# Optimization experiments

Hardware: AMD Instinct MI355X
Metric: run time of the kernel (lower is better)

Reference implementation:

```python
import jax, jax.numpy as jnp
import numpy as np


def _bilinear_sample(fea, px, py):
    # fea: [C,H,W]; px,py: [D,H,W] pixel coords (align_corners=True, zeros padding)
    C, H, W = fea.shape
    x0 = jnp.floor(px); y0 = jnp.floor(py)
    wx = px - x0; wy = py - y0
    x0i = x0.astype(jnp.int32); y0i = y0.astype(jnp.int32)

    def g(xi, yi):
        valid = (xi >= 0) & (xi < W) & (yi >= 0) & (yi < H)
        v = fea[:, jnp.clip(yi, 0, H - 1), jnp.clip(xi, 0, W - 1)]  # [C,D,H,W]
        return jnp.where(valid[None], v, 0.0)

    return (g(x0i, y0i) * ((1 - wx) * (1 - wy))[None]
            + g(x0i + 1, y0i) * (wx * (1 - wy))[None]
            + g(x0i, y0i + 1) * ((1 - wx) * wy)[None]
            + g(x0i + 1, y0i + 1) * (wx * wy)[None])


def homo_warping_3d(src_fea, src_proj, ref_proj, depth_values):
    # src_fea [B,C,H,W]; src_proj/ref_proj [B,4,4]; depth_values [B,D] -> [B,C,D,H,W]
    B, C, H, W = src_fea.shape
    D = depth_values.shape[1]
    proj = src_proj @ jnp.linalg.inv(ref_proj)
    rot, trans = proj[:, :3, :3], proj[:, :3, 3]
    yy, xx = jnp.meshgrid(jnp.arange(H, dtype=src_fea.dtype),
                          jnp.arange(W, dtype=src_fea.dtype), indexing='ij')
    xyz = jnp.stack([xx.ravel(), yy.ravel(), jnp.ones(H * W, src_fea.dtype)], 0)  # [3,HW]
    rot_xyz = jnp.einsum('bij,jp->bip', rot, xyz)  # [B,3,HW]
    pxyz = rot_xyz[:, :, None, :] * depth_values[:, None, :, None] + trans[:, :, None, None]
    xy = pxyz[:, :2] / pxyz[:, 2:3]
    # grid is computed under torch.no_grad() in the original
    px = jax.lax.stop_gradient(xy[:, 0].reshape(B, D, H, W))
    py = jax.lax.stop_gradient(xy[:, 1].reshape(B, D, H, W))
    return jax.vmap(_bilinear_sample)(src_fea, px, py)  # [B,C,D,H,W]


def conf_regression(p, n=4):
    # sliding sum of n consecutive depth probabilities, gathered at expected depth index
    B, D, H, W = p.shape
    pad = jnp.pad(p, ((0, 0), (1, 2), (0, 0), (0, 0)))  # [B,D+3,H,W]
    cs = jnp.cumsum(pad, axis=1)
    cs = jnp.concatenate([jnp.zeros_like(cs[:, :1]), cs], axis=1)  # [B,D+4,H,W]
    sum_n = cs[:, n:n + D] - cs[:, 0:D]  # [B,D,H,W]
    d_idx = jnp.sum(p * jnp.arange(D, dtype=p.dtype)[None, :, None, None], axis=1)
    idx = jnp.clip(d_idx.astype(jnp.int32), 0, D - 1)
    return jnp.take_along_axis(sum_n, idx[:, None], axis=1)[:, 0]


def reference(ref_feats, src_feats, proj_matrices, depth_values, num_depth, w_reg):
    V = proj_matrices.shape[1]
    assert ref_feats.shape[0] == V - 1 and depth_values.shape[1] == num_depth
    ref_proj = proj_matrices[:, 0]
    ref_proj_new = ref_proj[:, 0].at[:, :3, :4].set(ref_proj[:, 1, :3, :3] @ ref_proj[:, 0, :3, :4])
    volume_sum = 0.0
    for v in range(V - 1):
        src_proj = proj_matrices[:, v + 1]
        src_proj_new = src_proj[:, 0].at[:, :3, :4].set(src_proj[:, 1, :3, :3] @ src_proj[:, 0, :3, :4])
        warped = homo_warping_3d(src_feats[v], src_proj_new, ref_proj_new, depth_values)
        volume_sum = volume_sum + ref_feats[v][:, :, None] * warped  # [B,C,D,H,W]
    volume_mean = volume_sum / (V - 1)
    # cost regularization: bias-free 3x3x3 3D conv C->1
    cost = jax.lax.conv_general_dilated(volume_mean, w_reg, (1, 1, 1), 'SAME',
                                        dimension_numbers=('NCDHW', 'OIDHW', 'NCDHW'))
    prob_volume = jax.nn.softmax(cost[:, 0], axis=1)  # [B,D,H,W]
    depth = jnp.sum(prob_volume * depth_values[:, :, None, None], axis=1)  # [B,H,W]
    conf = jax.lax.stop_gradient(conf_regression(prob_volume))  # [B,H,W]
    return depth, conf


def setup_inputs() -> dict:
    key = jax.random.key(0)
    B, V, C, D, H, W = 1, 5, 32, 48, 128, 160
    k1, k2, k3 = jax.random.split(key, 3)
    ref_feats = jax.random.normal(k1, (V - 1, B, C, H, W), jnp.float32)
    src_feats = jax.random.normal(k2, (V - 1, B, C, H, W), jnp.float32)
    # geometrically valid cameras: index 0 = extrinsic 4x4, index 1 = intrinsic 4x4
    f = 200.0
    K = np.eye(4, dtype=np.float32)
    K[0, 0] = f; K[1, 1] = f; K[0, 2] = W / 2.0; K[1, 2] = H / 2.0
    projs = np.zeros((B, V, 2, 4, 4), np.float32)
    for v in range(V):
        ang = 0.04 * v
        R = np.array([[np.cos(ang), 0, np.sin(ang)], [0, 1, 0], [-np.sin(ang), 0, np.cos(ang)]], np.float32)
        E = np.eye(4, dtype=np.float32)
        E[:3, :3] = R
        E[:3, 3] = np.array([-40.0 * v, 0.0, 0.0], np.float32)
        projs[:, v, 0] = E
        projs[:, v, 1] = K
    depth_values = jnp.broadcast_to(jnp.linspace(425.0, 935.0, D, dtype=jnp.float32)[None], (B, D))
    w_reg = jax.random.normal(k3, (1, C, 3, 3, 3), jnp.float32) * 0.05
    return {"ref_feats": ref_feats, "src_feats": src_feats,
            "proj_matrices": jnp.asarray(projs), "depth_values": depth_values,
            "num_depth": D, "w_reg": w_reg}
```

## Files before the change

kernel.cpp:

```cpp
#include <hip/hip_runtime.h>
#include <math.h>

#define H_ 128
#define W_ 160
#define D_ 48
#define C_ 32
#define K27 27
#define HW_ (H_ * W_)
#define DHW_ (D_ * HW_)
#define CHW_ (C_ * HW_)

typedef float f4 __attribute__((ext_vector_type(4)));

__device__ __forceinline__ void build_proj(const float* __restrict__ P, int v,
                                           double M[4][4]) {
    const float* E = P + (v * 2 + 0) * 16;
    const float* K = P + (v * 2 + 1) * 16;
    for (int i = 0; i < 3; i++)
        for (int j = 0; j < 4; j++) {
            double s = 0.0;
            for (int k = 0; k < 3; k++) s += (double)K[i * 4 + k] * (double)E[k * 4 + j];
            M[i][j] = s;
        }
    for (int j = 0; j < 4; j++) M[3][j] = (double)E[12 + j];
}

__device__ void do_proj(const float* __restrict__ P, float* __restrict__ rt) {
    double M0[4][4];
    build_proj(P, 0, M0);
    double a[4][8];
    for (int i = 0; i < 4; i++)
        for (int j = 0; j < 4; j++) {
            a[i][j] = M0[i][j];
            a[i][4 + j] = (i == j) ? 1.0 : 0.0;
        }
    for (int col = 0; col < 4; ++col) {
        int piv = col;
        double best = fabs(a[col][col]);
        for (int r = col + 1; r < 4; r++) {
            double vv = fabs(a[r][col]);
            if (vv > best) { best = vv; piv = r; }
        }
        if (piv != col)
            for (int j = 0; j < 8; j++) {
                double t = a[col][j]; a[col][j] = a[piv][j]; a[piv][j] = t;
            }
        double inv = 1.0 / a[col][col];
        for (int j = 0; j < 8; j++) a[col][j] *= inv;
        for (int r = 0; r < 4; r++)
            if (r != col) {
                double f = a[r][col];
                for (int j = 0; j < 8; j++) a[r][j] -= f * a[col][j];
            }
    }
    double Minv[4][4];
    for (int i = 0; i < 4; i++)
        for (int j = 0; j < 4; j++) Minv[i][j] = a[i][4 + j];

    for (int v = 1; v < 5; ++v) {
        double Mv[4][4];
        build_proj(P, v, Mv);
        double Pm[4][4];
        for (int i = 0; i < 4; i++)
            for (int j = 0; j < 4; j++) {
                double s = 0.0;
                for (int k = 0; k < 4; k++) s += Mv[i][k] * Minv[k][j];
                Pm[i][j] = s;
            }
        float* o = rt + (v - 1) * 12;
        o[0] = (float)Pm[0][0]; o[1] = (float)Pm[0][1]; o[2] = (float)Pm[0][2];
        o[3] = (float)Pm[1][0]; o[4] = (float)Pm[1][1]; o[5] = (float)Pm[1][2];
        o[6] = (float)Pm[2][0]; o[7] = (float)Pm[2][1]; o[8] = (float)Pm[2][2];
        o[9] = (float)Pm[0][3]; o[10] = (float)Pm[1][3]; o[11] = (float)Pm[2][3];
    }
}

__global__ void __launch_bounds__(256)
transpose2_kernel(const float* __restrict__ sf, const float* __restrict__ rf,
                  float* __restrict__ so, float* __restrict__ ro,
                  const float* __restrict__ P, float* __restrict__ rt) {
    int blk = blockIdx.x;
    if (blk >= 2560) {
        if (threadIdx.x == 0) do_proj(P, rt);
        return;
    }
    __shared__ float tile[C_][65];
    int t = threadIdx.x;
    int tv = blk / 320;
    int tileI = blk % 320;
    int pixbase = tileI * 64;
    const float* in = (tv < 4) ? sf : rf;
    float* out = (tv < 4) ? so : ro;
    int v = tv & 3;

    int pix = t & 63;
    int cbase = (t >> 6) * 8;
#pragma unroll
    for (int cc = 0; cc < 8; cc++) {
        int c = cbase + cc;
        tile[c][pix] = in[(size_t)v * CHW_ + c * HW_ + pixbase + pix];
    }
    __syncthreads();

    float* obase = out + ((size_t)v * HW_ + pixbase) * C_;
#pragma unroll
    for (int r = 0; r < 2; r++) {
        int i = r * 256 + t;
        int wpix = i >> 3;
        int c0 = (i & 7) * 4;
        f4 w = {tile[c0][wpix], tile[c0 + 1][wpix], tile[c0 + 2][wpix],
                tile[c0 + 3][wpix]};
        *(f4*)(obase + (size_t)wpix * C_ + c0) = w;
    }
}

__global__ void __launch_bounds__(256)
warp_fold_x_kernel(const float* __restrict__ srcT,
                   const float* __restrict__ refT,
                   const float* __restrict__ rt,
                   const float* __restrict__ dvals,
                   const float* __restrict__ wreg,
                   float* __restrict__ Gx) {
    __shared__ float accT[8][64][4];
    __shared__ float gLDS[K27][164];

    int t = threadIdx.x;
    int vox = t >> 2;
    int cgrp = t & 3;
    int blk = blockIdx.x;
    int d = blk >> 7;
    int y = blk & 127;
    float depth = dvals[d];
    float yf = (float)y;
    int rowbase = d * HW_ + y * W_;

#pragma unroll 1
    for (int b = 0; b < 3; b++) {
        int vg = b * 64 + vox;
        int x = vg - 1;

        f4 acc0 = (f4){0.f, 0.f, 0.f, 0.f};
        f4 acc1 = (f4){0.f, 0.f, 0.f, 0.f};

        if (x >= 0 && x < W_) {
            float xf = (float)x;
            int pix = y * W_ + x;
#pragma unroll 2
            for (int v = 0; v < 4; v++) {
                const float* m = rt + v * 12;
                float px = fmaf(fmaf(m[0], xf, fmaf(m[1], yf, m[2])), depth, m[9]);
                float py = fmaf(fmaf(m[3], xf, fmaf(m[4], yf, m[5])), depth, m[10]);
                float pz = fmaf(fmaf(m[6], xf, fmaf(m[7], yf, m[8])), depth, m[11]);
                float iz = 1.f / pz;
                px *= iz;
                py *= iz;
                float x0f = floorf(px), y0f = floorf(py);
                float wx = px - x0f, wy = py - y0f;
                int x0 = (int)x0f, y0 = (int)y0f;
                int x1 = x0 + 1, y1 = y0 + 1;

                float w00 = (1.f - wx) * (1.f - wy);
                float w10 = wx * (1.f - wy);
                float w01 = (1.f - wx) * wy;
                float w11 = wx * wy;
                bool vx0 = (x0 >= 0) && (x0 < W_);
                bool vx1 = (x1 >= 0) && (x1 < W_);
                bool vy0 = (y0 >= 0) && (y0 < H_);
                bool vy1 = (y1 >= 0) && (y1 < H_);
                if (!(vx0 && vy0)) w00 = 0.f;
                if (!(vx1 && vy0)) w10 = 0.f;
                if (!(vx0 && vy1)) w01 = 0.f;
                if (!(vx1 && vy1)) w11 = 0.f;
                int cx0 = min(max(x0, 0), W_ - 1);
                int cx1 = min(max(x1, 0), W_ - 1);
                int cy0 = min(max(y0, 0), H_ - 1);
                int cy1 = min(max(y1, 0), H_ - 1);

                const float* sv = srcT + (size_t)v * HW_ * C_ + cgrp * 8;
                const f4* p00 = (const f4*)(sv + (cy0 * W_ + cx0) * C_);
                const f4* p10 = (const f4*)(sv + (cy0 * W_ + cx1) * C_);
                const f4* p01 = (const f4*)(sv + (cy1 * W_ + cx0) * C_);
                const f4* p11 = (const f4*)(sv + (cy1 * W_ + cx1) * C_);
                const f4* pr  = (const f4*)(refT + ((size_t)v * HW_ + pix) * C_ + cgrp * 8);

                f4 a00 = p00[0], b00 = p00[1];
                f4 a10 = p10[0], b10 = p10[1];
                f4 a01 = p01[0], b01 = p01[1];
                f4 a11 = p11[0], b11 = p11[1];
                f4 r0 = pr[0],  r1 = pr[1];

                f4 sv0 = a00 * w00 + a10 * w10 + a01 * w01 + a11 * w11;
                f4 sv1 = b00 * w00 + b10 * w10 + b01 * w01 + b11 * w11;
                acc0 += r0 * sv0;
                acc1 += r1 * sv1;
            }
            acc0 *= 0.25f;
            acc1 *= 0.25f;
        }

        int cq0 = cgrp * 2;
        *(f4*)&accT[cq0][vox][0] = acc0;
        *(f4*)&accT[cq0 + 1][vox][0] = acc1;
        __syncthreads();

        int fvox = t & 63;
        int kg = t >> 6;
        int fvg = b * 64 + fvox;
        float av[C_];
#pragma unroll
        for (int cq = 0; cq < 8; cq++)
            *(f4*)&av[cq * 4] = *(const f4*)&accT[cq][fvox][0];

        if (fvg < 162) {
            int kstart = kg * 7;
            int kend = min(kstart + 7, K27);
#pragma unroll 1
            for (int k = kstart; k < kend; k++) {
                int ku = __builtin_amdgcn_readfirstlane(k);
                float g = 0.f;
#pragma unroll
                for (int c = 0; c < C_; c++) g = fmaf(wreg[c * K27 + ku], av[c], g);
                gLDS[ku][fvg] = g;
            }
        }
        __syncthreads();
    }

    if (t < W_) {
        int x = t;
#pragma unroll
        for (int j = 0; j < 9; j++) {
            float s = gLDS[j * 3 + 0][x] + gLDS[j * 3 + 1][x + 1] +
                      gLDS[j * 3 + 2][x + 2];
            Gx[(size_t)j * DHW_ + rowbase + x] = s;
        }
    }
}

__global__ void __launch_bounds__(512)
gather_softmax_kernel(const float* __restrict__ Gx,
                      const float* __restrict__ dvals,
                      float* __restrict__ out) {
    __shared__ float E[D_][64];
    __shared__ float red[8][64];
    __shared__ float sums[3][8][64];

    int t = threadIdx.x;
    int lx = t & 63;
    int dg = t >> 6;
    int blk = blockIdx.x;
    int xt = blk % 3;
    int y = blk / 3;
    int x = xt * 64 + lx;
    bool xv = x < W_;
    int xc = min(x, W_ - 1);
    int dbase = dg * 6 - 1;

    float S0[8], S1[8], S2[8];
#pragma unroll
    for (int jj = 0; jj < 8; jj++) {
        float s0 = 0.f, s1 = 0.f, s2 = 0.f;
        int dp = dbase + jj;
        if ((unsigned)dp < (unsigned)D_) {
            const float* g0 = Gx + (size_t)dp * HW_ + xc;
#pragma unroll
            for (int kh = 0; kh < 3; kh++) {
                int yy = y + kh - 1;
                if ((unsigned)yy < (unsigned)H_) {
                    const float* gp = g0 + yy * W_ + (size_t)kh * DHW_;
                    s0 += gp[0];
                    s1 += *(gp + (size_t)3 * DHW_);
                    s2 += *(gp + (size_t)6 * DHW_);
                }
            }
        }
        S0[jj] = s0; S1[jj] = s1; S2[jj] = s2;
    }

    float cost[6];
    float lmax = -1e30f;
#pragma unroll
    for (int j = 0; j < 6; j++) {
        cost[j] = S0[j] + S1[j + 1] + S2[j + 2];
        lmax = fmaxf(lmax, cost[j]);
    }
    red[dg][lx] = lmax;
    __syncthreads();
    float mx = red[0][lx];
#pragma unroll
    for (int g = 1; g < 8; g++) mx = fmaxf(mx, red[g][lx]);

    float s = 0.f, dn = 0.f, din = 0.f;
#pragma unroll
    for (int j = 0; j < 6; j++) {
        int dd = dg * 6 + j;
        float e = __expf(cost[j] - mx);
        E[dd][lx] = e;
        s += e;
        dn = fmaf(e, dvals[dd], dn);
        din = fmaf(e, (float)dd, din);
    }
    sums[0][dg][lx] = s;
    sums[1][dg][lx] = dn;
    sums[2][dg][lx] = din;
    __syncthreads();

    if (dg == 0 && xv) {
        float S = 0.f, DN = 0.f, DI = 0.f;
#pragma unroll
        for (int g = 0; g < 8; g++) {
            S += sums[0][g][lx];
            DN += sums[1][g][lx];
            DI += sums[2][g][lx];
        }
        float invs = 1.f / S;
        float depth = DN * invs;
        int id = (int)(DI * invs);
        id = min(max(id, 0), D_ - 1);
        float conf = 0.f;
#pragma unroll 1
        for (int k = id - 1; k <= id + 2; ++k)
            if (k >= 0 && k < D_) conf += E[k][lx];
        int pix = y * W_ + x;
        out[pix] = depth;
        out[HW_ + pix] = conf * invs;
    }
}

extern "C" void kernel_launch(void* const* d_in, const int* in_sizes, int n_in,
                              void* d_out, int out_size, void* d_ws, size_t ws_size,
                              hipStream_t stream) {
    const float* ref_feats = (const float*)d_in[0];
    const float* src_feats = (const float*)d_in[1];
    const float* proj      = (const float*)d_in[2];
    const float* dvals     = (const float*)d_in[3];
    const float* wreg      = (const float*)d_in[5];
    float* out = (float*)d_out;

    char* ws = (char*)d_ws;
    float* rt   = (float*)ws;
    float* srcT = (float*)(ws + 1024);
    float* refT = srcT + (size_t)4 * HW_ * C_;
    float* Gx   = refT + (size_t)4 * HW_ * C_;

    transpose2_kernel<<<2561, 256, 0, stream>>>(src_feats, ref_feats, srcT, refT,
                                                proj, rt);
    warp_fold_x_kernel<<<D_ * H_, 256, 0, stream>>>(srcT, refT, rt, dvals, wreg, Gx);
    gather_softmax_kernel<<<3 * H_, 512, 0, stream>>>(Gx, dvals, out);
}
```

Baseline: 222.6 us.

## Shrink warp-fold LDS with per-chunk haloed output and split FMA chains

The warp/fold kernel now processes each row as three overlapping 64-voxel chunks with a stride of 62 and writes the x-folded output after every chunk. This cuts the gLDS buffer from 164 to 64 columns, and the launch bound asks for 8 blocks per CU to raise occupancy. The 32-channel weight dot product is split into four independent accumulators to shorten the dependency chain. The projection setup replaces the 4x4 Gauss-Jordan inverse with a closed-form 3x3 affine inverse. The trade-off is some redundant halo computation and an extra barrier per chunk.

```diff
diff --git a/kernel.cpp b/kernel.cpp
--- a/kernel.cpp
+++ b/kernel.cpp
@@ -12,66 +12,55 @@
 
 typedef float f4 __attribute__((ext_vector_type(4)));
 
-__device__ __forceinline__ void build_proj(const float* __restrict__ P, int v,
-                                           double M[4][4]) {
-    const float* E = P + (v * 2 + 0) * 16;
-    const float* K = P + (v * 2 + 1) * 16;
-    for (int i = 0; i < 3; i++)
-        for (int j = 0; j < 4; j++) {
+__device__ __forceinline__ void build_affine(const float* __restrict__ P, int v,
+                                             double A[3][3], double b[3]) {
+    const float* E = P + v * 32;
+    const float* K = P + v * 32 + 16;
+    for (int i = 0; i < 3; i++) {
+        for (int j = 0; j < 3; j++) {
             double s = 0.0;
             for (int k = 0; k < 3; k++) s += (double)K[i * 4 + k] * (double)E[k * 4 + j];
-            M[i][j] = s;
-        }
-    for (int j = 0; j < 4; j++) M[3][j] = (double)E[12 + j];
+            A[i][j] = s;
+        }
+        double s = 0.0;
+        for (int k = 0; k < 3; k++) s += (double)K[i * 4 + k] * (double)E[k * 4 + 3];
+        b[i] = s;
+    }
 }
 
 __device__ void do_proj(const float* __restrict__ P, float* __restrict__ rt) {
-    double M0[4][4];
-    build_proj(P, 0, M0);
-    double a[4][8];
-    for (int i = 0; i < 4; i++)
-        for (int j = 0; j < 4; j++) {
-            a[i][j] = M0[i][j];
-            a[i][4 + j] = (i == j) ? 1.0 : 0.0;
-        }
-    for (int col = 0; col < 4; ++col) {
-        int piv = col;
-        double best = fabs(a[col][col]);
-        for (int r = col + 1; r < 4; r++) {
-            double vv = fabs(a[r][col]);
-            if (vv > best) { best = vv; piv = r; }
-        }
-        if (piv != col)
-            for (int j = 0; j < 8; j++) {
-                double t = a[col][j]; a[col][j] = a[piv][j]; a[piv][j] = t;
-            }
-        double inv = 1.0 / a[col][col];
-        for (int j = 0; j < 8; j++) a[col][j] *= inv;
-        for (int r = 0; r < 4; r++)
-            if (r != col) {
-                double f = a[r][col];
-                for (int j = 0; j < 8; j++) a[r][j] -= f * a[col][j];
-            }
-    }
-    double Minv[4][4];
-    for (int i = 0; i < 4; i++)
-        for (int j = 0; j < 4; j++) Minv[i][j] = a[i][4 + j];
+    double A0[3][3], b0[3];
+    build_affine(P, 0, A0, b0);
+    double det = A0[0][0] * (A0[1][1] * A0[2][2] - A0[1][2] * A0[2][1])
+               - A0[0][1] * (A0[1][0] * A0[2][2] - A0[1][2] * A0[2][0])
+               + A0[0][2] * (A0[1][0] * A0[2][1] - A0[1][1] * A0[2][0]);
+    double id = 1.0 / det;
+    double Ai[3][3];
+    Ai[0][0] = (A0[1][1] * A0[2][2] - A0[1][2] * A0[2][1]) * id;
+    Ai[0][1] = (A0[0][2] * A0[2][1] - A0[0][1] * A0[2][2]) * id;
+    Ai[0][2] = (A0[0][1] * A0[1][2] - A0[0][2] * A0[1][1]) * id;
+    Ai[1][0] = (A0[1][2] * A0[2][0] - A0[1][0] * A0[2][2]) * id;
+    Ai[1][1] = (A0[0][0] * A0[2][2] - A0[0][2] * A0[2][0]) * id;
+    Ai[1][2] = (A0[0][2] * A0[1][0] - A0[0][0] * A0[1][2]) * id;
+    Ai[2][0] = (A0[1][0] * A0[2][1] - A0[1][1] * A0[2][0]) * id;
+    Ai[2][1] = (A0[0][1] * A0[2][0] - A0[0][0] * A0[2][1]) * id;
+    Ai[2][2] = (A0[0][0] * A0[1][1] - A0[0][1] * A0[1][0]) * id;
+    double t0[3];
+    for (int i = 0; i < 3; i++)
+        t0[i] = -(Ai[i][0] * b0[0] + Ai[i][1] * b0[1] + Ai[i][2] * b0[2]);
 
     for (int v = 1; v < 5; ++v) {
-        double Mv[4][4];
-        build_proj(P, v, Mv);
-        double Pm[4][4];
-        for (int i = 0; i < 4; i++)
-            for (int j = 0; j < 4; j++) {
-                double s = 0.0;
-                for (int k = 0; k < 4; k++) s += Mv[i][k] * Minv[k][j];
-                Pm[i][j] = s;
-            }
+        double Av[3][3], bv[3];
+        build_affine(P, v, Av, bv);
         float* o = rt + (v - 1) * 12;
-        o[0] = (float)Pm[0][0]; o[1] = (float)Pm[0][1]; o[2] = (float)Pm[0][2];
-        o[3] = (float)Pm[1][0]; o[4] = (float)Pm[1][1]; o[5] = (float)Pm[1][2];
-        o[6] = (float)Pm[2][0]; o[7] = (float)Pm[2][1]; o[8] = (float)Pm[2][2];
-        o[9] = (float)Pm[0][3]; o[10] = (float)Pm[1][3]; o[11] = (float)Pm[2][3];
+        for (int i = 0; i < 3; i++) {
+            for (int j = 0; j < 3; j++) {
+                double s = Av[i][0] * Ai[0][j] + Av[i][1] * Ai[1][j] + Av[i][2] * Ai[2][j];
+                o[i * 3 + j] = (float)s;
+            }
+            o[9 + i] = (float)(Av[i][0] * t0[0] + Av[i][1] * t0[1] +
+                               Av[i][2] * t0[2] + bv[i]);
+        }
     }
 }
 
@@ -114,7 +103,7 @@
     }
 }
 
-__global__ void __launch_bounds__(256)
+__global__ void __launch_bounds__(256, 8)
 warp_fold_x_kernel(const float* __restrict__ srcT,
                    const float* __restrict__ refT,
                    const float* __restrict__ rt,
@@ -122,7 +111,7 @@
                    const float* __restrict__ wreg,
                    float* __restrict__ Gx) {
     __shared__ float accT[8][64][4];
-    __shared__ float gLDS[K27][164];
+    __shared__ float gLDS[K27][64];
 
     int t = threadIdx.x;
     int vox = t >> 2;
@@ -136,8 +125,8 @@
 
 #pragma unroll 1
     for (int b = 0; b < 3; b++) {
-        int vg = b * 64 + vox;
-        int x = vg - 1;
+        int xbase = b * 62 - 1;
+        int x = xbase + vox;
 
         f4 acc0 = (f4){0.f, 0.f, 0.f, 0.f};
         f4 acc1 = (f4){0.f, 0.f, 0.f, 0.f};
@@ -205,35 +194,39 @@
 
         int fvox = t & 63;
         int kg = t >> 6;
-        int fvg = b * 64 + fvox;
         float av[C_];
 #pragma unroll
         for (int cq = 0; cq < 8; cq++)
             *(f4*)&av[cq * 4] = *(const f4*)&accT[cq][fvox][0];
 
-        if (fvg < 162) {
-            int kstart = kg * 7;
-            int kend = min(kstart + 7, K27);
+        int kstart = kg * 7;
+        int kend = min(kstart + 7, K27);
 #pragma unroll 1
-            for (int k = kstart; k < kend; k++) {
-                int ku = __builtin_amdgcn_readfirstlane(k);
-                float g = 0.f;
-#pragma unroll
-                for (int c = 0; c < C_; c++) g = fmaf(wreg[c * K27 + ku], av[c], g);
-                gLDS[ku][fvg] = g;
-            }
+        for (int k = kstart; k < kend; k++) {
+            int ku = __builtin_amdgcn_readfirstlane(k);
+            const float* wk = wreg + ku;
+            float g0 = 0.f, g1 = 0.f, g2 = 0.f, g3 = 0.f;
+#pragma unroll
+            for (int cq = 0; cq < 8; cq++) {
+                g0 = fmaf(wk[(cq * 4 + 0) * K27], av[cq * 4 + 0], g0);
+                g1 = fmaf(wk[(cq * 4 + 1) * K27], av[cq * 4 + 1], g1);
+                g2 = fmaf(wk[(cq * 4 + 2) * K27], av[cq * 4 + 2], g2);
+                g3 = fmaf(wk[(cq * 4 + 3) * K27], av[cq * 4 + 3], g3);
+            }
+            gLDS[ku][fvox] = (g0 + g1) + (g2 + g3);
         }
         __syncthreads();
-    }
-
-    if (t < W_) {
-        int x = t;
-#pragma unroll
-        for (int j = 0; j < 9; j++) {
-            float s = gLDS[j * 3 + 0][x] + gLDS[j * 3 + 1][x + 1] +
-                      gLDS[j * 3 + 2][x + 2];
-            Gx[(size_t)j * DHW_ + rowbase + x] = s;
-        }
+
+        int xout = b * 62 + t;
+        if (t < 62 && xout < W_) {
+#pragma unroll
+            for (int j = 0; j < 9; j++) {
+                float s = gLDS[j * 3 + 0][t] + gLDS[j * 3 + 1][t + 1] +
+                          gLDS[j * 3 + 2][t + 2];
+                Gx[(size_t)j * DHW_ + rowbase + xout] = s;
+            }
+        }
+        __syncthreads();
     }
 }
 
```

After: 239.8 us. 7.7% more time.
